# Kernel optimization log

Hardware: AMD Instinct MI355X
Metric: run time of the kernel (lower is better)

The kernel has to match this reference:

```python
import jax, jax.numpy as jnp
import numpy as np

EMBED = 1024
HEADS = 16
HEAD_SIZE = 64


def setup_inputs() -> dict:
    key = jax.random.key(0)
    ks = jax.random.split(key, 6)
    B, T = 2, 2048
    s = EMBED ** -0.5
    x = jax.random.normal(ks[0], (B, T, EMBED), dtype=jnp.float32)
    Wk = jax.random.normal(ks[1], (EMBED, HEADS * HEAD_SIZE), dtype=jnp.float32) * s
    Wq = jax.random.normal(ks[2], (EMBED, HEADS * HEAD_SIZE), dtype=jnp.float32) * s
    Wv = jax.random.normal(ks[3], (EMBED, HEADS * HEAD_SIZE), dtype=jnp.float32) * s
    Wp = jax.random.normal(ks[4], (HEADS * HEAD_SIZE, EMBED), dtype=jnp.float32) * s
    bp = jax.random.normal(ks[5], (EMBED,), dtype=jnp.float32) * 0.01
    return {"x": x, "Wk": Wk, "Wq": Wq, "Wv": Wv, "Wp": Wp, "bp": bp}


def reference(x, Wk, Wq, Wv, Wp, bp):
    # x: [B, T, C]; dropout in eval mode (identity), matching inference semantics
    B, T, C = x.shape
    def split_heads(y):  # [B,T,H*Dh] -> [B,H,T,Dh]
        return y.reshape(B, T, HEADS, HEAD_SIZE).transpose(0, 2, 1, 3)
    q = split_heads(x @ Wq)
    k = split_heads(x @ Wk)
    v = split_heads(x @ Wv)
    scale = HEAD_SIZE ** -0.5
    wei = jnp.einsum('bhqd,bhkd->bhqk', q, k) * scale  # [B,H,T,T]
    causal = jnp.tril(jnp.ones((T, T), dtype=bool))
    wei = jnp.where(causal, wei, -jnp.inf)
    wei = jax.nn.softmax(wei, axis=-1)
    out = jnp.einsum('bhqk,bhkd->bhqd', wei, v)  # [B,H,T,Dh]
    out = out.transpose(0, 2, 1, 3).reshape(B, T, HEADS * HEAD_SIZE)
    return out @ Wp + bp
```

## Files before the change

kernel.cpp:

```cpp
#include <hip/hip_runtime.h>
#include <stdint.h>


typedef unsigned short bfu;
typedef unsigned int u32;
typedef short bf16x8 __attribute__((ext_vector_type(8)));
typedef float f32x4 __attribute__((ext_vector_type(4)));
typedef float f32x16 __attribute__((ext_vector_type(16)));

#define DEVI static __device__ __forceinline__

DEVI bfu f2bf(float f) {
  union { float f; unsigned u; } a; a.f = f;
  unsigned u = a.u;
  u += 0x7fffu + ((u >> 16) & 1u);
  return (bfu)(u >> 16);
}

DEVI float bf2f(bfu x) {
  union { u32 u; float f; } a; a.u = ((u32)x) << 16; return a.f;
}

DEVI void gld_lds16(const void* g, void* l) {
  __builtin_amdgcn_global_load_lds(
      (const __attribute__((address_space(1))) void*)g,
      (__attribute__((address_space(3))) void*)l, 16, 0, 0);
}

#define BAR_VM4()                                         \
  do {                                                    \
    asm volatile("s_waitcnt vmcnt(4)" ::: "memory");      \
    __builtin_amdgcn_s_barrier();                         \
    asm volatile("" ::: "memory");                        \
  } while (0)
#define BAR_VM0()                                         \
  do {                                                    \
    asm volatile("s_waitcnt vmcnt(0)" ::: "memory");      \
    __builtin_amdgcn_s_barrier();                         \
    asm volatile("" ::: "memory");                        \
  } while (0)


__global__ __launch_bounds__(256) void conv_x(const float* __restrict__ x,
                                              bfu* __restrict__ xb) {
  const int n4 = (4096 * 1024) / 4;
  for (int i = blockIdx.x * 256 + threadIdx.x; i < n4; i += gridDim.x * 256) {
    float4 v = ((const float4*)x)[i];
    ushort4 p;
    p.x = f2bf(v.x); p.y = f2bf(v.y); p.z = f2bf(v.z); p.w = f2bf(v.w);
    ((ushort4*)xb)[i] = p;
  }
}

__global__ __launch_bounds__(256) void conv_w(
    const float* __restrict__ W0, const float* __restrict__ W1,
    const float* __restrict__ W2, const float* __restrict__ W3,
    bfu* __restrict__ T0, bfu* __restrict__ T1,
    bfu* __restrict__ T2, bfu* __restrict__ T3) {
  __shared__ bfu tile[64][65];
  const float* W; bfu* T;
  switch (blockIdx.z) {
    case 0:  W = W0; T = T0; break;
    case 1:  W = W1; T = T1; break;
    case 2:  W = W2; T = T2; break;
    default: W = W3; T = T3; break;
  }
  const int k0 = blockIdx.y * 64, n0 = blockIdx.x * 64;
  const int c = threadIdx.x & 63, r4 = threadIdx.x >> 6;
#pragma unroll
  for (int i = 0; i < 16; i++) {
    int row = r4 + i * 4;
    tile[row][c] = f2bf(W[(size_t)(k0 + row) * 1024 + n0 + c]);
  }
  __syncthreads();
#pragma unroll
  for (int i = 0; i < 16; i++) {
    int row = r4 + i * 4;
    T[(size_t)(n0 + row) * 1024 + k0 + c] = tile[c][row];
  }
}


__global__ __launch_bounds__(512) void gemm_qkv256(
    const bfu* __restrict__ A, const bfu* __restrict__ Bt,
    bfu* __restrict__ Qb, bfu* __restrict__ Kb, bfu* __restrict__ Vb) {
  __shared__ __align__(16) bfu LDS[2 * 32768];
  const int bid = blockIdx.x;
  const int xcd = bid & 7, i0 = bid >> 3;
  const int tx = i0 >> 1, ty = xcd * 2 + (i0 & 1);
  const int z = tx >> 2;
  const int m0 = ty * 256, n0g = tx * 256;
  const int tid = threadIdx.x, wave = tid >> 6, lane = tid & 63;
  const int wr = wave >> 2, wc = wave & 3;
  const int fr = lane & 15, fq = lane >> 4;
  const int rslot4 = fq ^ ((fr >> 1) & 3);

#define STAGE_HT(bufn, ktile, isB, kk)                                           \
  do {                                                                           \
    const bfu* srcb = (isB) ? Bt + (size_t)n0g * 1024 : A + (size_t)m0 * 1024;   \
    bfu* dstb = LDS + (bufn) * 32768 + ((isB) ? 16384 : 0) + (kk) * 8192;        \
    _Pragma("unroll")                                                            \
    for (int j_ = 0; j_ < 2; j_++) {                                             \
      int s_ = tid + j_ * 512;                                                   \
      int r_ = s_ >> 2, cg_ = (s_ & 3) ^ ((r_ >> 1) & 3);                        \
      gld_lds16(srcb + (size_t)r_ * 1024 + (ktile) * 64 + (kk) * 32 + cg_ * 8,   \
                dstb + s_ * 8);                                                  \
    }                                                                            \
  } while (0)

#define READ_B(kk)                                                               \
  _Pragma("unroll")                                                              \
  for (int n = 0; n < 4; n++)                                                    \
    bfv[n] = *(const bf16x8*)&bufc_p[16384 + (kk) * 8192 +                       \
              ((wc * 64 + n * 16 + fr) * 4 + rslot4) * 8];

#define READ_A(dst, mq, kk)                                                      \
  _Pragma("unroll")                                                              \
  for (int mm = 0; mm < 4; mm++)                                                 \
    dst[mm] = *(const bf16x8*)&bufc_p[(kk) * 8192 +                              \
              ((wr * 128 + ((mq) * 4 + mm) * 16 + fr) * 4 + rslot4) * 8];

#define MFMA_Q(afv, mq)                                                          \
  __builtin_amdgcn_s_setprio(1);                                                 \
  _Pragma("unroll")                                                              \
  for (int mm = 0; mm < 4; mm++)                                                 \
    _Pragma("unroll")                                                            \
    for (int n = 0; n < 4; n++)                                                  \
      acc[(mq) * 4 + mm][n] = __builtin_amdgcn_mfma_f32_16x16x32_bf16(           \
          afv[mm], bfv[n], acc[(mq) * 4 + mm][n], 0, 0, 0);                      \
  __builtin_amdgcn_s_setprio(0);

  f32x4 acc[8][4] = {};
  STAGE_HT(0, 0, 0, 0);
  STAGE_HT(0, 0, 1, 0);
  STAGE_HT(0, 0, 0, 1);
  STAGE_HT(0, 0, 1, 1);
  BAR_VM4();

  const int NT = 16;
  for (int t = 0; t < NT; t++) {
    const int more = (t + 1 < NT);
    const bfu* bufc_p = LDS + (t & 1) * 32768;
    const int bufn = (t & 1) ^ 1;
    bf16x8 bfv[4], afA[4], afB[4];
    READ_B(0);
    READ_A(afA, 0, 0);
    if (more) STAGE_HT(bufn, t + 1, 0, 0);
    MFMA_Q(afA, 0);
    READ_A(afB, 1, 0);
    if (more) STAGE_HT(bufn, t + 1, 1, 0);
    MFMA_Q(afB, 1);
    if (more) BAR_VM4();
    else      BAR_VM0();
    READ_B(1);
    READ_A(afA, 0, 1);
    if (more) STAGE_HT(bufn, t + 1, 0, 1);
    MFMA_Q(afA, 0);
    READ_A(afB, 1, 1);
    if (more) STAGE_HT(bufn, t + 1, 1, 1);
    MFMA_Q(afB, 1);
    BAR_VM4();
  }
#undef STAGE_HT
#undef READ_B
#undef READ_A
#undef MFMA_Q

  const float qs = (z == 0) ? 0.1803368801f : 1.0f;
#pragma unroll
  for (int mf = 0; mf < 8; mf++)
#pragma unroll
    for (int n = 0; n < 4; n++) {
      int r = m0 + wr * 128 + mf * 16 + fq * 4;
      int cwm = (tx & 3) * 256 + wc * 64 + n * 16 + fr;
      int b = r >> 11, tt = r & 2047, h = cwm >> 6, d = cwm & 63;
      if (z == 0) {
        size_t base = ((size_t)(b * 16 + h) * 2048 + tt) * 64 + d;
#pragma unroll
        for (int i = 0; i < 4; i++)
          Qb[base + (size_t)i * 64] = f2bf(acc[mf][n][i] * qs);
      } else if (z == 1) {
        size_t base = ((size_t)(b * 16 + h) * 2048 + tt) * 64 + d;
#pragma unroll
        for (int i = 0; i < 4; i++)
          Kb[base + (size_t)i * 64] = f2bf(acc[mf][n][i]);
      } else {
        size_t base = ((size_t)(b * 16 + h) * 64 + d) * 2048 + tt;
        ushort4 p;
        p.x = f2bf(acc[mf][n][0]); p.y = f2bf(acc[mf][n][1]);
        p.z = f2bf(acc[mf][n][2]); p.w = f2bf(acc[mf][n][3]);
        *(ushort4*)&Vb[base] = p;
      }
    }
}


DEVI void gemm128_core(const bfu* __restrict__ A, const bfu* __restrict__ Bt,
                       int K, int m0, int n0, bfu* As, bfu* Bs, int tid,
                       f32x4 acc[4][4]) {
  const int lane = tid & 63, wave = tid >> 6;
  const int wr = wave >> 1, wc = wave & 1;
  const int fr = lane & 15, fq = lane >> 4;
  const int r_a = tid >> 2;
  const int koff = ((tid & 3) ^ ((tid >> 3) & 3)) * 8;
  const int rslot = (fq ^ ((fr >> 1) & 3)) * 8;
#define GSTAGE(buf, k0s)                                                              \
  do {                                                                                \
    gld_lds16(A  + (size_t)(m0 +      r_a) * K + (k0s) + koff,                        \
              As + (buf) * 4096 + tid * 8);                                           \
    gld_lds16(A  + (size_t)(m0 + 64 + r_a) * K + (k0s) + koff,                        \
              As + (buf) * 4096 + 2048 + tid * 8);                                    \
    gld_lds16(Bt + (size_t)(n0 +      r_a) * K + (k0s) + koff,                        \
              Bs + (buf) * 4096 + tid * 8);                                           \
    gld_lds16(Bt + (size_t)(n0 + 64 + r_a) * K + (k0s) + koff,                        \
              Bs + (buf) * 4096 + 2048 + tid * 8);                                    \
  } while (0)
  const int NS = K >> 5;
  GSTAGE(0, 0);
  GSTAGE(1, 32);
  BAR_VM4();
  for (int i = 0; i < NS; i++) {
    if (i + 2 < NS) GSTAGE((i + 2) % 3, (i + 2) * 32);
    const bfu* AsC = As + (i % 3) * 4096;
    const bfu* BsC = Bs + (i % 3) * 4096;
    bf16x8 af[4], bfv[4];
#pragma unroll
    for (int m = 0; m < 4; m++)
      af[m] = *(const bf16x8*)&AsC[(wr * 64 + m * 16 + fr) * 32 + rslot];
#pragma unroll
    for (int n = 0; n < 4; n++)
      bfv[n] = *(const bf16x8*)&BsC[(wc * 64 + n * 16 + fr) * 32 + rslot];
#pragma unroll
    for (int m = 0; m < 4; m++)
#pragma unroll
      for (int n = 0; n < 4; n++)
        acc[m][n] = __builtin_amdgcn_mfma_f32_16x16x32_bf16(af[m], bfv[n],
                                                            acc[m][n], 0, 0, 0);
    if (i + 2 < NS) BAR_VM4();
    else            BAR_VM0();
  }
#undef GSTAGE
}

__global__ __launch_bounds__(256) void gemm_proj(
    const bfu* __restrict__ A, const bfu* __restrict__ Bt,
    const float* __restrict__ bias, float* __restrict__ out) {
  __shared__ __align__(16) bfu As[3 * 4096];
  __shared__ __align__(16) bfu Bs[3 * 4096];
  const int bid = blockIdx.x;
  const int xcd = bid & 7, i0 = bid >> 3;
  const int tx = i0 >> 2, ty = xcd * 4 + (i0 & 3);
  const int m0 = ty * 128, n0 = tx * 128;
  const int tid = threadIdx.x, lane = tid & 63, wave = tid >> 6;
  const int wr = wave >> 1, wc = wave & 1, fr = lane & 15, fq = lane >> 4;
  f32x4 acc[4][4] = {};
  gemm128_core(A, Bt, 1024, m0, n0, As, Bs, tid, acc);
#pragma unroll
  for (int m = 0; m < 4; m++)
#pragma unroll
    for (int n = 0; n < 4; n++) {
      int r = m0 + wr * 64 + m * 16 + fq * 4;
      int c = n0 + wc * 64 + n * 16 + fr;
      float bv = bias[c];
#pragma unroll
      for (int i = 0; i < 4; i++)
        out[(size_t)(r + i) * 1024 + c] = acc[m][n][i] + bv;
    }
}


__global__ __launch_bounds__(256) void attn_fwd(
    const bfu* __restrict__ Q, const bfu* __restrict__ K,
    const bfu* __restrict__ Vt, bfu* __restrict__ Ob,
    bfu* __restrict__ PO, float* __restrict__ PM, float* __restrict__ PL) {
  __shared__ __align__(16) bfu Ks[2][64 * 64];
  __shared__ __align__(16) bfu Vs[2][64 * 64];
  const int bid = blockIdx.x;
  const int xcd = bid & 7, i0 = bid >> 3;
  const int slot = i0 >> 5, cuL = i0 & 31;
  const int head = cuL >> 3, cu8 = cuL & 7;
  const int hb = xcd * 4 + head;
  int qb, mode;
  if (slot < 2)      { qb = 15 - cu8; mode = slot + 1; }
  else if (cu8 < 4)  { if (slot == 3) return; qb = cu8; mode = 0; }
  else               { qb = cu8; mode = slot - 1; }
  const int kb0   = (mode == 2) ? (qb + 1) : 0;
  const int kbmax = (mode == 1) ? qb : (2 * qb + 1);
  const int tid = threadIdx.x, wave = tid >> 6, lane = tid & 63;
  const int q31 = lane & 31, hi = lane >> 5;
  const bfu* Qh = Q  + (size_t)hb * 2048 * 64;
  const bfu* Kh = K  + (size_t)hb * 2048 * 64;
  const bfu* Vh = Vt + (size_t)hb * 64 * 2048;
  const int b = hb >> 4, h = hb & 15;
  const int q0w = qb * 128 + wave * 32;
  const int qg = q0w + q31;

  const int r0 = tid >> 3, r1 = (256 + tid) >> 3;
  const int c0 = (tid & 7) ^ (r0 & 7), c1 = (tid & 7) ^ (r1 & 7);
#define STAGE(bufi, kbase)                                                            \
  do {                                                                                \
    gld_lds16(Kh + (size_t)((kbase) + r0) * 64 + c0 * 8, &Ks[bufi][tid * 8]);         \
    gld_lds16(Kh + (size_t)((kbase) + r1) * 64 + c1 * 8, &Ks[bufi][(256 + tid) * 8]); \
    gld_lds16(Vh + (size_t)r0 * 2048 + (kbase) + c0 * 8, &Vs[bufi][tid * 8]);         \
    gld_lds16(Vh + (size_t)r1 * 2048 + (kbase) + c1 * 8, &Vs[bufi][(256 + tid) * 8]); \
  } while (0)

  bf16x8 qv[4];
#pragma unroll
  for (int c = 0; c < 4; c++)
    qv[c] = *(const bf16x8*)&Qh[(size_t)(q0w + q31) * 64 + c * 16 + hi * 8];

  bf16x8 onesv;
#pragma unroll
  for (int j = 0; j < 8; j++) onesv[j] = (short)0x3F80;

  f32x16 o0 = {}, o1 = {}, lac = {};
  float m = -1e30f;

  STAGE(0, kb0 * 64);
  __syncthreads();

  int cc = 0;
  for (int kb = kb0; kb <= kbmax; kb++, cc ^= 1) {
    const int cur = cc;
    if (kb < kbmax) STAGE(cur ^ 1, (kb + 1) * 64);
    const int kbase = kb * 64;
    if (kbase <= q0w + 31) {
      const bfu* KsC = Ks[cur];
      const bfu* VsC = Vs[cur];
      f32x16 s0 = {}, s1 = {};
#pragma unroll
      for (int c = 0; c < 4; c++) {
        const int g = 2 * c + hi;
        bf16x8 kf0 = *(const bf16x8*)&KsC[(q31 * 8 + (g ^ (q31 & 7))) * 8];
        bf16x8 kf1 = *(const bf16x8*)&KsC[((32 + q31) * 8 + (g ^ (q31 & 7))) * 8];
        s0 = __builtin_amdgcn_mfma_f32_32x32x16_bf16(kf0, qv[c], s0, 0, 0, 0);
        s1 = __builtin_amdgcn_mfma_f32_32x32x16_bf16(kf1, qv[c], s1, 0, 0, 0);
      }
      if (kbase + 63 > q0w) {
#pragma unroll
        for (int r = 0; r < 16; r++) {
          int krow = (r & 3) + 8 * (r >> 2) + 4 * hi;
          if (kbase + krow > qg)      s0[r] = -1e30f;
          if (kbase + 32 + krow > qg) s1[r] = -1e30f;
        }
      }
      float pm = s0[0];
#pragma unroll
      for (int r = 1; r < 16; r++) pm = fmaxf(pm, s0[r]);
#pragma unroll
      for (int r = 0; r < 16; r++) pm = fmaxf(pm, s1[r]);
      pm = fmaxf(pm, __shfl_xor(pm, 32));
      if (!__all(pm <= m + 8.0f)) {
        float mn = fmaxf(m, pm);
        float al = __builtin_amdgcn_exp2f(m - mn);
        m = mn;
#pragma unroll
        for (int r = 0; r < 16; r++) {
          float alq = __shfl(al, (r & 3) + 8 * (r >> 2) + 4 * hi);
          o0[r] *= alq; o1[r] *= alq; lac[r] *= alq;
        }
      }
      u32 W0[8], W1[8];
#pragma unroll
      for (int w = 0; w < 8; w++) {
        float a0 = __builtin_amdgcn_exp2f(s0[2 * w] - m);
        float a1 = __builtin_amdgcn_exp2f(s0[2 * w + 1] - m);
        asm("v_cvt_pk_bf16_f32 %0, %1, %2" : "=v"(W0[w]) : "v"(a0), "v"(a1));
        float b0 = __builtin_amdgcn_exp2f(s1[2 * w] - m);
        float b1 = __builtin_amdgcn_exp2f(s1[2 * w + 1] - m);
        asm("v_cvt_pk_bf16_f32 %0, %1, %2" : "=v"(W1[w]) : "v"(b0), "v"(b1));
      }
      __builtin_amdgcn_s_setprio(1);
#pragma unroll
      for (int c = 0; c < 4; c++) {
        const u32* Wsel = (c < 2) ? W0 : W1;
        const int w0 = 4 * (c & 1);
        u32 t0 = Wsel[w0],     t2 = Wsel[w0 + 2];
        u32 t1 = Wsel[w0 + 1], t3 = Wsel[w0 + 3];
        asm("v_permlane32_swap_b32 %0, %1" : "+v"(t0), "+v"(t2));
        asm("v_permlane32_swap_b32 %0, %1" : "+v"(t1), "+v"(t3));
        union { u32 u[4]; bf16x8 v; } pa;
        pa.u[0] = t0; pa.u[1] = t1; pa.u[2] = t2; pa.u[3] = t3;
        const int g = 2 * c + hi;
        bf16x8 vb0 = *(const bf16x8*)&VsC[(q31 * 8 + (g ^ (q31 & 7))) * 8];
        bf16x8 vb1 = *(const bf16x8*)&VsC[((32 + q31) * 8 + (g ^ (q31 & 7))) * 8];
        o0  = __builtin_amdgcn_mfma_f32_32x32x16_bf16(pa.v, vb0,   o0,  0, 0, 0);
        o1  = __builtin_amdgcn_mfma_f32_32x32x16_bf16(pa.v, vb1,   o1,  0, 0, 0);
        lac = __builtin_amdgcn_mfma_f32_32x32x16_bf16(pa.v, onesv, lac, 0, 0, 0);
      }
      __builtin_amdgcn_s_setprio(0);
    }
    __syncthreads();
  }
#undef STAGE

  if (mode == 0) {
#pragma unroll
    for (int r = 0; r < 16; r++) {
      int t = q0w + (r & 3) + 8 * (r >> 2) + 4 * hi;
      float inv = 1.0f / lac[r];
      size_t base = (size_t)(b * 2048 + t) * 1024 + h * 64;
      Ob[base + q31]      = f2bf(o0[r] * inv);
      Ob[base + 32 + q31] = f2bf(o1[r] * inv);
    }
  } else {
    const int p = (hb * 12 + (qb - 4)) * 2 + (mode - 1);
    bfu*   po = PO + (size_t)p * 8192;
    float* pmv = PM + p * 128;
    float* plv = PL + p * 128;
    pmv[wave * 32 + q31] = m;
#pragma unroll
    for (int r = 0; r < 16; r++) {
      int rm = (r & 3) + 8 * (r >> 2) + 4 * hi;
      plv[wave * 32 + rm] = lac[r];
      po[(wave * 32 + rm) * 64 + q31]      = f2bf(o0[r]);
      po[(wave * 32 + rm) * 64 + 32 + q31] = f2bf(o1[r]);
    }
  }
}

__global__ __launch_bounds__(256) void attn_comb(
    const bfu* __restrict__ PO, const float* __restrict__ PM,
    const float* __restrict__ PL, bfu* __restrict__ Ob) {
  const int g = blockIdx.x;
  const int hb = g / 12, j = g % 12, qb = j + 4;
  const int b = hb >> 4, h = hb & 15;
  const int p0 = g * 2, p1 = p0 + 1;
  const int tid = threadIdx.x;
  const int r = tid >> 1, ch = tid & 1;
  float m0 = PM[p0 * 128 + r], m1 = PM[p1 * 128 + r];
  float l0 = PL[p0 * 128 + r], l1 = PL[p1 * 128 + r];
  float ms = fmaxf(m0, m1);
  float f0 = __builtin_amdgcn_exp2f(m0 - ms);
  float f1 = __builtin_amdgcn_exp2f(m1 - ms);
  float inv = 1.0f / (l0 * f0 + l1 * f1);
  const bfu* a0 = PO + (size_t)p0 * 8192 + r * 64 + ch * 32;
  const bfu* a1 = PO + (size_t)p1 * 8192 + r * 64 + ch * 32;
  const int t = qb * 128 + r;
  bfu* ob = Ob + (size_t)(b * 2048 + t) * 1024 + h * 64 + ch * 32;
#pragma unroll
  for (int k = 0; k < 4; k++) {
    bf16x8 v0 = *(const bf16x8*)(a0 + k * 8);
    bf16x8 v1 = *(const bf16x8*)(a1 + k * 8);
    bf16x8 vo;
#pragma unroll
    for (int e = 0; e < 8; e++) {
      float acc = bf2f((bfu)(unsigned short)v0[e]) * f0 +
                  bf2f((bfu)(unsigned short)v1[e]) * f1;
      vo[e] = (short)f2bf(acc * inv);
    }
    *(bf16x8*)(ob + k * 8) = vo;
  }
}


extern "C" void kernel_launch(void* const* d_in, const int* in_sizes, int n_in,
                              void* d_out, int out_size, void* d_ws, size_t ws_size,
                              hipStream_t stream) {
  const float* x  = (const float*)d_in[0];
  const float* Wk = (const float*)d_in[1];
  const float* Wq = (const float*)d_in[2];
  const float* Wv = (const float*)d_in[3];
  const float* Wp = (const float*)d_in[4];
  const float* bp = (const float*)d_in[5];
  char* ws = (char*)d_ws;
  bfu* xb  = (bfu*)(ws);
  bfu* Wqt = (bfu*)(ws + ( 8u << 20));
  bfu* Wkt = (bfu*)(ws + (10u << 20));
  bfu* Wvt = (bfu*)(ws + (12u << 20));
  bfu* Wpt = (bfu*)(ws + (14u << 20));
  bfu* Qb  = (bfu*)(ws + (16u << 20));
  bfu* Kb  = (bfu*)(ws + (24u << 20));
  bfu* Vb  = (bfu*)(ws + (32u << 20));
  bfu* Ab  = (bfu*)(ws + (40u << 20));
  bfu*   PO = (bfu*)(ws);
  float* PM = (float*)(ws + (13u << 20));
  float* PL = (float*)(ws + (13u << 20) + (512u << 10));
  float* out = (float*)d_out;

  conv_x<<<1024, 256, 0, stream>>>(x, xb);
  conv_w<<<dim3(16, 16, 4), 256, 0, stream>>>(Wq, Wk, Wv, Wp, Wqt, Wkt, Wvt, Wpt);
  gemm_qkv256<<<192, 512, 0, stream>>>(xb, Wqt, Qb, Kb, Vb);
  attn_fwd<<<1024, 256, 0, stream>>>(Qb, Kb, Vb, Ab, PO, PM, PL);
  attn_comb<<<384, 256, 0, stream>>>(PO, PM, PL, Ab);
  gemm_proj<<<256, 256, 0, stream>>>(Ab, Wpt, bp, out);
}
```

Measured before the change: 121.7 us.

## Triple-buffer K/V tiles with distance-2 prefetch and split K/V staging

Moves the attention kernel's K/V LDS staging from double to triple buffering, so loads are issued two key blocks ahead. K and V loads for the next-next block are issued at different points in the loop body: K before QK^T and V after softmax. The full __syncthreads is replaced with vmcnt-based barriers (BAR_VM4/BAR_VM0), which wait only for the older loads to finish. This hides more global-load latency but raises LDS use from 32KB to 48KB per block, which may reduce occupancy.

```diff
diff --git a/kernel.cpp b/kernel.cpp
--- a/kernel.cpp
+++ b/kernel.cpp
@@ -273,8 +273,8 @@
     const bfu* __restrict__ Q, const bfu* __restrict__ K,
     const bfu* __restrict__ Vt, bfu* __restrict__ Ob,
     bfu* __restrict__ PO, float* __restrict__ PM, float* __restrict__ PL) {
-  __shared__ __align__(16) bfu Ks[2][64 * 64];
-  __shared__ __align__(16) bfu Vs[2][64 * 64];
+  __shared__ __align__(16) bfu Ks[3][4096];
+  __shared__ __align__(16) bfu Vs[3][4096];
   const int bid = blockIdx.x;
   const int xcd = bid & 7, i0 = bid >> 3;
   const int slot = i0 >> 5, cuL = i0 & 31;
@@ -297,10 +297,13 @@
 
   const int r0 = tid >> 3, r1 = (256 + tid) >> 3;
   const int c0 = (tid & 7) ^ (r0 & 7), c1 = (tid & 7) ^ (r1 & 7);
-#define STAGE(bufi, kbase)                                                            \
+#define STAGE_K(bufi, kbase)                                                          \
   do {                                                                                \
     gld_lds16(Kh + (size_t)((kbase) + r0) * 64 + c0 * 8, &Ks[bufi][tid * 8]);         \
     gld_lds16(Kh + (size_t)((kbase) + r1) * 64 + c1 * 8, &Ks[bufi][(256 + tid) * 8]); \
+  } while (0)
+#define STAGE_V(bufi, kbase)                                                          \
+  do {                                                                                \
     gld_lds16(Vh + (size_t)r0 * 2048 + (kbase) + c0 * 8, &Vs[bufi][tid * 8]);         \
     gld_lds16(Vh + (size_t)r1 * 2048 + (kbase) + c1 * 8, &Vs[bufi][(256 + tid) * 8]); \
   } while (0)
@@ -317,17 +320,23 @@
   f32x16 o0 = {}, o1 = {}, lac = {};
   float m = -1e30f;
 
-  STAGE(0, kb0 * 64);
-  __syncthreads();
-
-  int cc = 0;
-  for (int kb = kb0; kb <= kbmax; kb++, cc ^= 1) {
-    const int cur = cc;
-    if (kb < kbmax) STAGE(cur ^ 1, (kb + 1) * 64);
+  STAGE_K(0, kb0 * 64);
+  STAGE_V(0, kb0 * 64);
+  STAGE_K(1, (kb0 + 1) * 64);
+  STAGE_V(1, (kb0 + 1) * 64);
+  BAR_VM4();
+
+  for (int kb = kb0; kb <= kbmax; kb++) {
+    const int idx = kb - kb0;
+    const int cur = idx % 3, nxt = (idx + 2) % 3;
+    const int pre = (kb + 2 <= kbmax);
     const int kbase = kb * 64;
-    if (kbase <= q0w + 31) {
-      const bfu* KsC = Ks[cur];
-      const bfu* VsC = Vs[cur];
+    const int active = (kbase <= q0w + 31);
+    const bfu* KsC = Ks[cur];
+    const bfu* VsC = Vs[cur];
+    if (pre) STAGE_K(nxt, (kb + 2) * 64);
+    u32 W0[8], W1[8];
+    if (active) {
       f32x16 s0 = {}, s1 = {};
 #pragma unroll
       for (int c = 0; c < 4; c++) {
@@ -361,7 +370,6 @@
           o0[r] *= alq; o1[r] *= alq; lac[r] *= alq;
         }
       }
-      u32 W0[8], W1[8];
 #pragma unroll
       for (int w = 0; w < 8; w++) {
         float a0 = __builtin_amdgcn_exp2f(s0[2 * w] - m);
@@ -371,6 +379,9 @@
         float b1 = __builtin_amdgcn_exp2f(s1[2 * w + 1] - m);
         asm("v_cvt_pk_bf16_f32 %0, %1, %2" : "=v"(W1[w]) : "v"(b0), "v"(b1));
       }
+    }
+    if (pre) STAGE_V(nxt, (kb + 2) * 64);
+    if (active) {
       __builtin_amdgcn_s_setprio(1);
 #pragma unroll
       for (int c = 0; c < 4; c++) {
@@ -391,9 +402,11 @@
       }
       __builtin_amdgcn_s_setprio(0);
     }
-    __syncthreads();
-  }
-#undef STAGE
+    if (pre) BAR_VM4();
+    else     BAR_VM0();
+  }
+#undef STAGE_K
+#undef STAGE_V
 
   if (mode == 0) {
 #pragma unroll
```

Result: no change. 121.1 us (-0.5%).
